# Performance work log

Hardware: AMD Instinct MI355X
Metric: run time of the kernel (lower is better)

## Reference

```python
import jax, jax.numpy as jnp
import numpy as np

NUM_LAYERS = 3
CHANNELS = 8
IN_CHANNELS = 8
MASK_OUT_STRIDE = 4
WEIGHT_NUMS = [(IN_CHANNELS + 2) * CHANNELS, CHANNELS * CHANNELS, CHANNELS]  # [80, 64, 8]
BIAS_NUMS = [CHANNELS, CHANNELS, 1]
NUM_GEN = sum(WEIGHT_NUMS) + sum(BIAS_NUMS)  # 169


def parse_params(params, weight_nums, bias_nums, channels):
    # params: [n_inst, sum(weight_nums)+sum(bias_nums)]
    n = params.shape[0]
    sizes = list(weight_nums) + list(bias_nums)
    splits = jnp.split(params, np.cumsum(sizes)[:-1].tolist(), axis=1)
    L = len(weight_nums)
    ws, bs = [], []
    for l in range(L):
        cout = channels if l < L - 1 else 1
        ws.append(splits[l].reshape(n, cout, -1))       # [n, cout, cin]
        bs.append(splits[L + l].reshape(n, cout))        # [n, cout]
    return ws, bs


def mask_head(x, ws, bs):
    # x: [n, cin, HW]; per-instance 1x1 convs == batched small GEMMs
    x_concat = None
    L = len(ws)
    for i, (w, b) in enumerate(zip(ws, bs)):
        x = jnp.einsum('noc,nch->noh', w, x) + b[:, :, None]
        if i < L - 1:
            x = jax.nn.relu(x)
        if i == L - 2:
            x_concat = x
    return x, x_concat


def aligned_bilinear(x, factor):
    # faithful port of AdelaiDet aligned_bilinear (align_corners=True interp)
    if factor == 1:
        return x
    n, c, h, w = x.shape
    x = jnp.pad(x, ((0, 0), (0, 0), (0, 1), (0, 1)), mode='edge')  # [h+1, w+1]
    oh, ow = factor * h + 1, factor * w + 1

    def interp_axis(arr, out_len, axis):
        # align_corners=True with out = factor*in - factor + 1 -> src = dst/factor exactly
        pos = jnp.arange(out_len) / factor
        i0 = jnp.floor(pos).astype(jnp.int32)
        i1 = jnp.minimum(i0 + 1, arr.shape[axis] - 1)
        frac = (pos - i0).astype(arr.dtype)
        a0 = jnp.take(arr, i0, axis=axis)
        a1 = jnp.take(arr, i1, axis=axis)
        shp = [1] * arr.ndim
        shp[axis] = out_len
        frac = frac.reshape(shp)
        return a0 * (1 - frac) + a1 * frac

    x = interp_axis(x, oh, 2)
    x = interp_axis(x, ow, 3)
    p = factor // 2
    x = jnp.pad(x, ((0, 0), (0, 0), (p, 0), (p, 0)), mode='edge')
    return x[:, :, :oh - 1, :ow - 1]


def setup_inputs() -> dict:
    key = jax.random.key(0)
    k1, k2, k3, k4, k5, k6 = jax.random.split(key, 6)
    N, Cin, H, W = 2, IN_CHANNELS, 100, 152
    n_inst = 128
    return {
        'mask_feats_body': jax.random.normal(k1, (N, Cin, H, W), dtype=jnp.float32),
        'mask_feats_edge': jax.random.normal(k2, (N, Cin, H, W), dtype=jnp.float32),
        'mask_head_params': jax.random.normal(k3, (n_inst, 2 * NUM_GEN + 81), dtype=jnp.float32) * 0.2,
        'inst_locations': jax.random.uniform(k4, (n_inst, 2), dtype=jnp.float32) * jnp.array([W * 8.0, H * 8.0]),
        'sizes_of_interest': jnp.array([64.0, 128.0, 256.0, 512.0, 1024.0], dtype=jnp.float32),
        'im_inds': jax.random.randint(k5, (n_inst,), 0, N, dtype=jnp.int32),
        'fpn_levels': jax.random.randint(k6, (n_inst,), 0, 5, dtype=jnp.int32),
        'mask_feat_stride': 8,
    }


def reference(mask_feats_body, mask_feats_edge, mask_head_params, inst_locations,
              sizes_of_interest, im_inds, fpn_levels, mask_feat_stride):
    N, Cin, H, W = mask_feats_body.shape
    n_inst = mask_head_params.shape[0]
    stride = mask_feat_stride

    # compute_locations: (x, y) grid at feature stride, offset stride//2
    shifts_x = jnp.arange(W, dtype=jnp.float32) * stride + stride // 2
    shifts_y = jnp.arange(H, dtype=jnp.float32) * stride + stride // 2
    sy, sx = jnp.meshgrid(shifts_y, shifts_x, indexing='ij')
    locations = jnp.stack([sx.reshape(-1), sy.reshape(-1)], axis=1)  # [HW, 2]

    rel = inst_locations[:, None, :] - locations[None, :, :]          # [n, HW, 2]
    rel = jnp.transpose(rel, (0, 2, 1))                               # [n, 2, HW]
    soi = sizes_of_interest[fpn_levels]                               # [n]
    rel = rel / soi[:, None, None]

    fb = mask_feats_body[im_inds].reshape(n_inst, Cin, H * W)
    fe = mask_feats_edge[im_inds].reshape(n_inst, Cin, H * W)
    inp_b = jnp.concatenate([rel, fb], axis=1)   # [n, Cin+2, HW]
    inp_e = jnp.concatenate([rel, fe], axis=1)

    wb, bb = parse_params(mask_head_params[:, :NUM_GEN], WEIGHT_NUMS, BIAS_NUMS, CHANNELS)
    we, be = parse_params(mask_head_params[:, NUM_GEN:2 * NUM_GEN], WEIGHT_NUMS, BIAS_NUMS, CHANNELS)
    wf, bf = parse_params(mask_head_params[:, 2 * NUM_GEN:], WEIGHT_NUMS[1:], BIAS_NUMS[1:], CHANNELS)

    logits_b, concat_b = mask_head(inp_b, wb, bb)
    logits_e, concat_e = mask_head(inp_e, we, be)
    logits_f, _ = mask_head(concat_b + concat_e, wf, bf)

    factor = mask_feat_stride // MASK_OUT_STRIDE
    outs = []
    for l in (logits_b, logits_e, logits_f):
        l = l.reshape(n_inst, 1, H, W)
        outs.append(jax.nn.sigmoid(aligned_bilinear(l, factor)))
    return tuple(outs)
```

## Files before the change

### kernel.cpp

```cpp
#include <hip/hip_runtime.h>
#include <hip/hip_bf16.h>
#include <hip/hip_fp16.h>

#define CIN      8
#define HH       100
#define WW       152
#define HWSZ     (HH * WW)
#define OHGT     200
#define OWID     304
#define PPI      419
#define OUT_PER_INST (OHGT * OWID)


typedef float vf4 __attribute__((ext_vector_type(4)));
typedef float vfloat4 __attribute__((ext_vector_type(4)));

__device__ __forceinline__ vf4 fma4(float w, vf4 x, vf4 a) { return w * x + a; }
__device__ __forceinline__ vf4 relu4(vf4 x) {
    vf4 r; r.x = fmaxf(x.x, 0.f); r.y = fmaxf(x.y, 0.f);
    r.z = fmaxf(x.z, 0.f); r.w = fmaxf(x.w, 0.f); return r;
}
__device__ __forceinline__ void store_h4(__half* dst, vf4 v) {
    union { __half2 h[2]; uint2 u; } pk;
    pk.h[0] = __floats2half2_rn(v.x, v.y);
    pk.h[1] = __floats2half2_rn(v.z, v.w);
    *(uint2*)dst = pk.u;
}

__global__ __launch_bounds__(256) void dmh_mlp4_kernel(
    const float* __restrict__ fbody,
    const float* __restrict__ fedge,
    const float* __restrict__ params,
    const float* __restrict__ locs,
    const float* __restrict__ soi_tab,
    const int*   __restrict__ im_inds,
    const int*   __restrict__ fpn_levels,
    __half* __restrict__ logits,
    int n_inst)
{
    const int n  = blockIdx.y;
    const int i  = blockIdx.x * 256 + threadIdx.x;
    const int px = 4 * i;
    if (px >= HWSZ) return;

    const float* __restrict__ p = params + (size_t)n * PPI;
    const int   im      = im_inds[n];
    const float inv_soi = 1.0f / soi_tab[fpn_levels[n]];
    const float sx = (locs[2 * n]     - 4.0f) * inv_soi;
    const float sy = (locs[2 * n + 1] - 4.0f) * inv_soi;
    const float k8 = 8.0f * inv_soi;

    const int r = px / WW;
    const int c = px - r * WW;
    const float dx0 = sx - (float)c * k8;
    const vf4 dx = { dx0, dx0 - k8, dx0 - 2.f * k8, dx0 - 3.f * k8 };
    const float dyv = sy - (float)r * k8;
    const vf4 dy = { dyv, dyv, dyv, dyv };

    const float* __restrict__ fb = fbody + (size_t)im * CIN * HWSZ + px;
    const float* __restrict__ fe = fedge + (size_t)im * CIN * HWSZ + px;

    vf4 in[10], h1[8];

    in[0] = dx; in[1] = dy;
    #pragma unroll
    for (int k = 0; k < 8; ++k)
        in[k + 2] = *(const vf4*)(fb + k * HWSZ);
    #pragma unroll
    for (int o = 0; o < 8; ++o) {
        vf4 a = p[152 + o];
        #pragma unroll
        for (int k = 0; k < 10; ++k) a = fma4(p[o * 10 + k], in[k], a);
        h1[o] = relu4(a);
    }
    vf4 h2b[8];
    #pragma unroll
    for (int o = 0; o < 8; ++o) {
        vf4 a = p[160 + o];
        #pragma unroll
        for (int k = 0; k < 8; ++k) a = fma4(p[80 + o * 8 + k], h1[k], a);
        h2b[o] = relu4(a);
    }
    vf4 lb = p[168];
    #pragma unroll
    for (int k = 0; k < 8; ++k) lb = fma4(p[144 + k], h2b[k], lb);

    #pragma unroll
    for (int k = 0; k < 8; ++k)
        in[k + 2] = *(const vf4*)(fe + k * HWSZ);
    #pragma unroll
    for (int o = 0; o < 8; ++o) {
        vf4 a = p[169 + 152 + o];
        #pragma unroll
        for (int k = 0; k < 10; ++k) a = fma4(p[169 + o * 10 + k], in[k], a);
        h1[o] = relu4(a);
    }
    vf4 h2e[8];
    #pragma unroll
    for (int o = 0; o < 8; ++o) {
        vf4 a = p[169 + 160 + o];
        #pragma unroll
        for (int k = 0; k < 8; ++k) a = fma4(p[169 + 80 + o * 8 + k], h1[k], a);
        h2e[o] = relu4(a);
    }
    vf4 le = p[169 + 168];
    #pragma unroll
    for (int k = 0; k < 8; ++k) le = fma4(p[169 + 144 + k], h2e[k], le);

    vf4 hs[8];
    #pragma unroll
    for (int k = 0; k < 8; ++k) hs[k] = h2b[k] + h2e[k];
    vf4 hf[8];
    #pragma unroll
    for (int o = 0; o < 8; ++o) {
        vf4 a = p[410 + o];
        #pragma unroll
        for (int k = 0; k < 8; ++k) a = fma4(p[338 + o * 8 + k], hs[k], a);
        hf[o] = relu4(a);
    }
    vf4 lf = p[418];
    #pragma unroll
    for (int k = 0; k < 8; ++k) lf = fma4(p[402 + k], hf[k], lf);

    const size_t hstride = (size_t)n_inst * HWSZ;
    __half* lg = logits + (size_t)n * HWSZ + px;
    store_h4(lg,               lb);
    store_h4(lg + hstride,     le);
    store_h4(lg + 2 * hstride, lf);
}

__global__ __launch_bounds__(256) void dmh_upsample_kernel(
    const __half* __restrict__ logits,
    float* __restrict__ out)
{
    int idx = blockIdx.x * 256 + threadIdx.x;
    const int q = idx % 76;  idx /= 76;
    const int r = idx % HH;  idx /= HH;

    const __half* __restrict__ L = logits + (size_t)idx * HWSZ + r * WW;
    float* __restrict__ O = out + (size_t)idx * OUT_PER_INST;

    const int cm = max(2 * q - 1, 0);
    const int c0 = 2 * q;
    const int cp = min(2 * q + 1, WW - 1);
    const int rpOff = (r < HH - 1) ? WW : 0;

    const float Lm0 = __half2float(L[cm]);
    const float L00 = __half2float(L[c0]);
    const float Lp0 = __half2float(L[cp]);
    const float Lm1 = __half2float(L[cm + rpOff]);
    const float L01 = __half2float(L[c0 + rpOff]);
    const float Lp1 = __half2float(L[cp + rpOff]);

    const float a0 = 0.5f * (Lm0 + L00);
    const float a1 = L00;
    const float a2 = 0.5f * (L00 + Lp0);
    const float a3 = Lp0;
    const float m  = 0.5f * (Lm0 + Lm1);
    const float z  = 0.5f * (L00 + L01);
    const float pz = 0.5f * (Lp0 + Lp1);
    const float b0 = 0.5f * (m + z);
    const float b1 = z;
    const float b2 = 0.5f * (z + pz);
    const float b3 = pz;

    vfloat4 A, B;
    A.x = 1.0f / (1.0f + __expf(-a0));
    A.y = 1.0f / (1.0f + __expf(-a1));
    A.z = 1.0f / (1.0f + __expf(-a2));
    A.w = 1.0f / (1.0f + __expf(-a3));
    B.x = 1.0f / (1.0f + __expf(-b0));
    B.y = 1.0f / (1.0f + __expf(-b1));
    B.z = 1.0f / (1.0f + __expf(-b2));
    B.w = 1.0f / (1.0f + __expf(-b3));

    const int xq = 4 * q;
    __builtin_nontemporal_store(A, (vfloat4*)(O + (size_t)(2 * r + 1) * OWID + xq));
    if (r == 0)
        __builtin_nontemporal_store(A, (vfloat4*)(O + xq));
    if (r < HH - 1)
        __builtin_nontemporal_store(B, (vfloat4*)(O + (size_t)(2 * r + 2) * OWID + xq));
}

extern "C" void kernel_launch(void* const* d_in, const int* in_sizes, int n_in,
                              void* d_out, int out_size, void* d_ws, size_t ws_size,
                              hipStream_t stream) {
    const float* fbody   = (const float*)d_in[0];
    const float* fedge   = (const float*)d_in[1];
    const float* params  = (const float*)d_in[2];
    const float* locs    = (const float*)d_in[3];
    const float* soi     = (const float*)d_in[4];
    const int*   im_inds = (const int*)d_in[5];
    const int*   fpn     = (const int*)d_in[6];

    const int n_inst = in_sizes[5];
    __half* logits = (__half*)d_ws;

    dim3 g1((HWSZ / 4 + 255) / 256, n_inst);
    dmh_mlp4_kernel<<<g1, dim3(256), 0, stream>>>(
        fbody, fedge, params, locs, soi, im_inds, fpn, logits, n_inst);

    const int total2 = 3 * n_inst * HH * 76;
    dmh_upsample_kernel<<<dim3(total2 / 256), dim3(256), 0, stream>>>(
        logits, (float*)d_out);
}
```

Before: 49.63 us.

## Fuse MLP and upsample into one kernel via shared-memory logit strips

Merges the per-pixel dynamic mask-head MLP and the aligned bilinear upsample plus sigmoid into a single kernel. Each block computes logits for a 5-row strip plus one halo row into shared memory, synchronises, then upsamples and writes the output. This removes the fp16 logits round trip through global memory and one kernel launch. In exchange, the halo row is recomputed per strip, only 228 of 256 threads do MLP work, and the barrier serialises compute and store phases within a block.

```diff
diff --git a/kernel.cpp b/kernel.cpp
--- a/kernel.cpp
+++ b/kernel.cpp
@@ -11,23 +11,23 @@
 #define PPI      419
 #define OUT_PER_INST (OHGT * OWID)
 
+#define RSTRIP   5
+#define TROWS    6
+#define NSTRIPS  20
+#define QPT      38
+#define P1THREADS (TROWS * QPT)
+#define P2ITEMS  (3 * RSTRIP * 76)
+
 
 typedef float vf4 __attribute__((ext_vector_type(4)));
-typedef float vfloat4 __attribute__((ext_vector_type(4)));
 
 __device__ __forceinline__ vf4 fma4(float w, vf4 x, vf4 a) { return w * x + a; }
 __device__ __forceinline__ vf4 relu4(vf4 x) {
     vf4 r; r.x = fmaxf(x.x, 0.f); r.y = fmaxf(x.y, 0.f);
     r.z = fmaxf(x.z, 0.f); r.w = fmaxf(x.w, 0.f); return r;
 }
-__device__ __forceinline__ void store_h4(__half* dst, vf4 v) {
-    union { __half2 h[2]; uint2 u; } pk;
-    pk.h[0] = __floats2half2_rn(v.x, v.y);
-    pk.h[1] = __floats2half2_rn(v.z, v.w);
-    *(uint2*)dst = pk.u;
-}
-
-__global__ __launch_bounds__(256) void dmh_mlp4_kernel(
+
+__global__ __launch_bounds__(256) void dmh_fused3_kernel(
     const float* __restrict__ fbody,
     const float* __restrict__ fedge,
     const float* __restrict__ params,
@@ -35,13 +35,15 @@
     const float* __restrict__ soi_tab,
     const int*   __restrict__ im_inds,
     const int*   __restrict__ fpn_levels,
-    __half* __restrict__ logits,
+    float* __restrict__ out,
     int n_inst)
 {
-    const int n  = blockIdx.y;
-    const int i  = blockIdx.x * 256 + threadIdx.x;
-    const int px = 4 * i;
-    if (px >= HWSZ) return;
+    const int s   = blockIdx.x;
+    const int n   = blockIdx.y;
+    const int tid = threadIdx.x;
+    const int r0  = RSTRIP * s;
+
+    __shared__ float slog[3][TROWS][WW];
 
     const float* __restrict__ p = params + (size_t)n * PPI;
     const int   im      = im_inds[n];
@@ -50,136 +52,132 @@
     const float sy = (locs[2 * n + 1] - 4.0f) * inv_soi;
     const float k8 = 8.0f * inv_soi;
 
-    const int r = px / WW;
-    const int c = px - r * WW;
-    const float dx0 = sx - (float)c * k8;
-    const vf4 dx = { dx0, dx0 - k8, dx0 - 2.f * k8, dx0 - 3.f * k8 };
-    const float dyv = sy - (float)r * k8;
-    const vf4 dy = { dyv, dyv, dyv, dyv };
-
-    const float* __restrict__ fb = fbody + (size_t)im * CIN * HWSZ + px;
-    const float* __restrict__ fe = fedge + (size_t)im * CIN * HWSZ + px;
-
-    vf4 in[10], h1[8];
-
-    in[0] = dx; in[1] = dy;
-    #pragma unroll
-    for (int k = 0; k < 8; ++k)
-        in[k + 2] = *(const vf4*)(fb + k * HWSZ);
-    #pragma unroll
-    for (int o = 0; o < 8; ++o) {
-        vf4 a = p[152 + o];
-        #pragma unroll
-        for (int k = 0; k < 10; ++k) a = fma4(p[o * 10 + k], in[k], a);
-        h1[o] = relu4(a);
+    if (tid < P1THREADS) {
+        const int rl = tid / QPT;
+        const int c  = (tid - rl * QPT) * 4;
+        const int r  = min(r0 + rl, HH - 1);
+        const int px = r * WW + c;
+
+        const float dx0 = sx - (float)c * k8;
+        const vf4 dx = { dx0, dx0 - k8, dx0 - 2.f * k8, dx0 - 3.f * k8 };
+        const float dyv = sy - (float)r * k8;
+        const vf4 dy = { dyv, dyv, dyv, dyv };
+
+        const float* __restrict__ fb = fbody + (size_t)im * CIN * HWSZ + px;
+        const float* __restrict__ fe = fedge + (size_t)im * CIN * HWSZ + px;
+
+        vf4 in[10], h1[8];
+
+        in[0] = dx; in[1] = dy;
+        #pragma unroll
+        for (int k = 0; k < 8; ++k)
+            in[k + 2] = *(const vf4*)(fb + k * HWSZ);
+        #pragma unroll
+        for (int o = 0; o < 8; ++o) {
+            vf4 a = p[152 + o];
+            #pragma unroll
+            for (int k = 0; k < 10; ++k) a = fma4(p[o * 10 + k], in[k], a);
+            h1[o] = relu4(a);
+        }
+        vf4 h2b[8];
+        #pragma unroll
+        for (int o = 0; o < 8; ++o) {
+            vf4 a = p[160 + o];
+            #pragma unroll
+            for (int k = 0; k < 8; ++k) a = fma4(p[80 + o * 8 + k], h1[k], a);
+            h2b[o] = relu4(a);
+        }
+        vf4 lb = p[168];
+        #pragma unroll
+        for (int k = 0; k < 8; ++k) lb = fma4(p[144 + k], h2b[k], lb);
+
+        #pragma unroll
+        for (int k = 0; k < 8; ++k)
+            in[k + 2] = *(const vf4*)(fe + k * HWSZ);
+        #pragma unroll
+        for (int o = 0; o < 8; ++o) {
+            vf4 a = p[169 + 152 + o];
+            #pragma unroll
+            for (int k = 0; k < 10; ++k) a = fma4(p[169 + o * 10 + k], in[k], a);
+            h1[o] = relu4(a);
+        }
+        vf4 h2e[8];
+        #pragma unroll
+        for (int o = 0; o < 8; ++o) {
+            vf4 a = p[169 + 160 + o];
+            #pragma unroll
+            for (int k = 0; k < 8; ++k) a = fma4(p[169 + 80 + o * 8 + k], h1[k], a);
+            h2e[o] = relu4(a);
+        }
+        vf4 le = p[169 + 168];
+        #pragma unroll
+        for (int k = 0; k < 8; ++k) le = fma4(p[169 + 144 + k], h2e[k], le);
+
+        vf4 hs[8];
+        #pragma unroll
+        for (int k = 0; k < 8; ++k) hs[k] = h2b[k] + h2e[k];
+        vf4 hf[8];
+        #pragma unroll
+        for (int o = 0; o < 8; ++o) {
+            vf4 a = p[410 + o];
+            #pragma unroll
+            for (int k = 0; k < 8; ++k) a = fma4(p[338 + o * 8 + k], hs[k], a);
+            hf[o] = relu4(a);
+        }
+        vf4 lf = p[418];
+        #pragma unroll
+        for (int k = 0; k < 8; ++k) lf = fma4(p[402 + k], hf[k], lf);
+
+        *(vf4*)&slog[0][rl][c] = lb;
+        *(vf4*)&slog[1][rl][c] = le;
+        *(vf4*)&slog[2][rl][c] = lf;
     }
-    vf4 h2b[8];
-    #pragma unroll
-    for (int o = 0; o < 8; ++o) {
-        vf4 a = p[160 + o];
-        #pragma unroll
-        for (int k = 0; k < 8; ++k) a = fma4(p[80 + o * 8 + k], h1[k], a);
-        h2b[o] = relu4(a);
+    __syncthreads();
+
+    for (int it = tid; it < P2ITEMS; it += 256) {
+        const int h   = it / (RSTRIP * 76);
+        const int rem = it - h * (RSTRIP * 76);
+        const int rr  = rem / 76;
+        const int q   = rem - rr * 76;
+        const int r   = r0 + rr;
+
+        const int cm = max(2 * q - 1, 0);
+        const int c0 = 2 * q;
+        const int cp = min(2 * q + 1, WW - 1);
+
+        const float Lm0 = slog[h][rr][cm],     L00 = slog[h][rr][c0],     Lp0 = slog[h][rr][cp];
+        const float Lm1 = slog[h][rr + 1][cm], L01 = slog[h][rr + 1][c0], Lp1 = slog[h][rr + 1][cp];
+
+        const float a0 = 0.5f * (Lm0 + L00);
+        const float a1 = L00;
+        const float a2 = 0.5f * (L00 + Lp0);
+        const float a3 = Lp0;
+        const float m  = 0.5f * (Lm0 + Lm1);
+        const float z  = 0.5f * (L00 + L01);
+        const float pz = 0.5f * (Lp0 + Lp1);
+        const float b0 = 0.5f * (m + z);
+        const float b1 = z;
+        const float b2 = 0.5f * (z + pz);
+        const float b3 = pz;
+
+        vf4 A, B;
+        A.x = 1.0f / (1.0f + __expf(-a0));
+        A.y = 1.0f / (1.0f + __expf(-a1));
+        A.z = 1.0f / (1.0f + __expf(-a2));
+        A.w = 1.0f / (1.0f + __expf(-a3));
+        B.x = 1.0f / (1.0f + __expf(-b0));
+        B.y = 1.0f / (1.0f + __expf(-b1));
+        B.z = 1.0f / (1.0f + __expf(-b2));
+        B.w = 1.0f / (1.0f + __expf(-b3));
+
+        float* __restrict__ O = out + ((size_t)h * n_inst + n) * OUT_PER_INST;
+        const int xq = 4 * q;
+        __builtin_nontemporal_store(A, (vf4*)(O + (size_t)(2 * r + 1) * OWID + xq));
+        if (r == 0)
+            __builtin_nontemporal_store(A, (vf4*)(O + xq));
+        if (r < HH - 1)
+            __builtin_nontemporal_store(B, (vf4*)(O + (size_t)(2 * r + 2) * OWID + xq));
     }
-    vf4 lb = p[168];
-    #pragma unroll
-    for (int k = 0; k < 8; ++k) lb = fma4(p[144 + k], h2b[k], lb);
-
-    #pragma unroll
-    for (int k = 0; k < 8; ++k)
-        in[k + 2] = *(const vf4*)(fe + k * HWSZ);
-    #pragma unroll
-    for (int o = 0; o < 8; ++o) {
-        vf4 a = p[169 + 152 + o];
-        #pragma unroll
-        for (int k = 0; k < 10; ++k) a = fma4(p[169 + o * 10 + k], in[k], a);
-        h1[o] = relu4(a);
-    }
-    vf4 h2e[8];
-    #pragma unroll
-    for (int o = 0; o < 8; ++o) {
-        vf4 a = p[169 + 160 + o];
-        #pragma unroll
-        for (int k = 0; k < 8; ++k) a = fma4(p[169 + 80 + o * 8 + k], h1[k], a);
-        h2e[o] = relu4(a);
-    }
-    vf4 le = p[169 + 168];
-    #pragma unroll
-    for (int k = 0; k < 8; ++k) le = fma4(p[169 + 144 + k], h2e[k], le);
-
-    vf4 hs[8];
-    #pragma unroll
-    for (int k = 0; k < 8; ++k) hs[k] = h2b[k] + h2e[k];
-    vf4 hf[8];
-    #pragma unroll
-    for (int o = 0; o < 8; ++o) {
-        vf4 a = p[410 + o];
-        #pragma unroll
-        for (int k = 0; k < 8; ++k) a = fma4(p[338 + o * 8 + k], hs[k], a);
-        hf[o] = relu4(a);
-    }
-    vf4 lf = p[418];
-    #pragma unroll
-    for (int k = 0; k < 8; ++k) lf = fma4(p[402 + k], hf[k], lf);
-
-    const size_t hstride = (size_t)n_inst * HWSZ;
-    __half* lg = logits + (size_t)n * HWSZ + px;
-    store_h4(lg,               lb);
-    store_h4(lg + hstride,     le);
-    store_h4(lg + 2 * hstride, lf);
-}
-
-__global__ __launch_bounds__(256) void dmh_upsample_kernel(
-    const __half* __restrict__ logits,
-    float* __restrict__ out)
-{
-    int idx = blockIdx.x * 256 + threadIdx.x;
-    const int q = idx % 76;  idx /= 76;
-    const int r = idx % HH;  idx /= HH;
-
-    const __half* __restrict__ L = logits + (size_t)idx * HWSZ + r * WW;
-    float* __restrict__ O = out + (size_t)idx * OUT_PER_INST;
-
-    const int cm = max(2 * q - 1, 0);
-    const int c0 = 2 * q;
-    const int cp = min(2 * q + 1, WW - 1);
-    const int rpOff = (r < HH - 1) ? WW : 0;
-
-    const float Lm0 = __half2float(L[cm]);
-    const float L00 = __half2float(L[c0]);
-    const float Lp0 = __half2float(L[cp]);
-    const float Lm1 = __half2float(L[cm + rpOff]);
-    const float L01 = __half2float(L[c0 + rpOff]);
-    const float Lp1 = __half2float(L[cp + rpOff]);
-
-    const float a0 = 0.5f * (Lm0 + L00);
-    const float a1 = L00;
-    const float a2 = 0.5f * (L00 + Lp0);
-    const float a3 = Lp0;
-    const float m  = 0.5f * (Lm0 + Lm1);
-    const float z  = 0.5f * (L00 + L01);
-    const float pz = 0.5f * (Lp0 + Lp1);
-    const float b0 = 0.5f * (m + z);
-    const float b1 = z;
-    const float b2 = 0.5f * (z + pz);
-    const float b3 = pz;
-
-    vfloat4 A, B;
-    A.x = 1.0f / (1.0f + __expf(-a0));
-    A.y = 1.0f / (1.0f + __expf(-a1));
-    A.z = 1.0f / (1.0f + __expf(-a2));
-    A.w = 1.0f / (1.0f + __expf(-a3));
-    B.x = 1.0f / (1.0f + __expf(-b0));
-    B.y = 1.0f / (1.0f + __expf(-b1));
-    B.z = 1.0f / (1.0f + __expf(-b2));
-    B.w = 1.0f / (1.0f + __expf(-b3));
-
-    const int xq = 4 * q;
-    __builtin_nontemporal_store(A, (vfloat4*)(O + (size_t)(2 * r + 1) * OWID + xq));
-    if (r == 0)
-        __builtin_nontemporal_store(A, (vfloat4*)(O + xq));
-    if (r < HH - 1)
-        __builtin_nontemporal_store(B, (vfloat4*)(O + (size_t)(2 * r + 2) * OWID + xq));
 }
 
 extern "C" void kernel_launch(void* const* d_in, const int* in_sizes, int n_in,
@@ -194,13 +192,9 @@
     const int*   fpn     = (const int*)d_in[6];
 
     const int n_inst = in_sizes[5];
-    __half* logits = (__half*)d_ws;
-
-    dim3 g1((HWSZ / 4 + 255) / 256, n_inst);
-    dmh_mlp4_kernel<<<g1, dim3(256), 0, stream>>>(
-        fbody, fedge, params, locs, soi, im_inds, fpn, logits, n_inst);
-
-    const int total2 = 3 * n_inst * HH * 76;
-    dmh_upsample_kernel<<<dim3(total2 / 256), dim3(256), 0, stream>>>(
-        logits, (float*)d_out);
+
+    dim3 grid(NSTRIPS, n_inst);
+    dmh_fused3_kernel<<<grid, dim3(256), 0, stream>>>(
+        fbody, fedge, params, locs, soi, im_inds, fpn,
+        (float*)d_out, n_inst);
 }
```

After: 42.61 us. 14.2% less time.
